# Optimization experiments

Measured on AMD Instinct MI355X. Metric: run time of the kernel, lower is better.

## Reference

```python
import jax, jax.numpy as jnp
import numpy as np

B, T, E = 8, 2048, 2048

def setup_inputs() -> dict:
    key = jax.random.key(0)
    k1, k2, k3 = jax.random.split(key, 3)
    x = jax.random.normal(k1, (B, T, E), dtype=jnp.float32)
    weight = jax.random.normal(k2, (T,), dtype=jnp.float32)
    bias = jax.random.normal(k3, (T,), dtype=jnp.float32)
    return {"x": x, "weight": weight, "bias": bias}

def _toeplitz_matrix(v, T):
    # M[i, j] = v[j - i] for j >= i, else 0  (upper-triangular Toeplitz)
    idx = jnp.arange(T)
    diff = idx[None, :] - idx[:, None]          # [T, T], diff = j - i
    M = jnp.where(diff >= 0, v[jnp.clip(diff, 0, T - 1)], jnp.zeros((), v.dtype))
    return M

def reference(x, weight, bias):
    Tlen = x.shape[1]
    W = _toeplitz_matrix(weight[:Tlen], Tlen).astype(x.dtype)  # [T, T]
    # original: out[b,e,t'] = sum_t x[b,e,t] * W[t,t']; in (B,T,E) layout:
    out = jnp.einsum('bte,ts->bse', x, W)
    out = out + bias[:Tlen][None, :, None]
    return out
```

## Files before the change

### kernel.cpp

```cpp
#include <hip/hip_runtime.h>
#include <hip/hip_bf16.h>

#define T_LEN 2048
#define E_LEN 2048
#define B_SZ  8
#define BM 128
#define BN 128
#define BK2 64
#define WREV_LEN 4104

typedef short short8 __attribute__((ext_vector_type(8)));
typedef float floatx4 __attribute__((ext_vector_type(4)));

typedef const __attribute__((address_space(1))) void* gas_ptr;
typedef __attribute__((address_space(3))) void* lds_ptr;

__global__ __launch_bounds__(256) void transpose_cast(
    const float* __restrict__ x, __hip_bfloat16* __restrict__ xT)
{
    const int t0 = blockIdx.x * 64, e0 = blockIdx.y * 64, b = blockIdx.z;
    __shared__ unsigned int W[64][33];
    const int tid = threadIdx.x;
    const int wave = tid >> 6, lane = tid & 63;

    const float* xb = x + (size_t)b * T_LEN * E_LEN;
    const int c = tid & 15;
    const int q = tid >> 4;

    #pragma unroll
    for (int i = 0; i < 2; ++i) {
        const int tp = q + 16 * i;
        const float4 a4 = *reinterpret_cast<const float4*>(
            xb + (size_t)(t0 + 2 * tp) * E_LEN + e0 + 4 * c);
        const float4 b4 = *reinterpret_cast<const float4*>(
            xb + (size_t)(t0 + 2 * tp + 1) * E_LEN + e0 + 4 * c);
        const float av[4] = {a4.x, a4.y, a4.z, a4.w};
        const float bv[4] = {b4.x, b4.y, b4.z, b4.w};
        #pragma unroll
        for (int j = 0; j < 4; ++j) {
            __hip_bfloat16 ha = __float2bfloat16(av[j]);
            __hip_bfloat16 hb = __float2bfloat16(bv[j]);
            unsigned int w =
                (unsigned int)*reinterpret_cast<unsigned short*>(&ha) |
                ((unsigned int)*reinterpret_cast<unsigned short*>(&hb) << 16);
            W[4 * c + j][tp] = w;
        }
    }
    __syncthreads();

    __hip_bfloat16* xTb = xT + (size_t)b * E_LEN * T_LEN;
    const int p = lane & 31;
    const int er = lane >> 5;
    #pragma unroll
    for (int i = 0; i < 8; ++i) {
        const int e = wave * 2 + i * 8 + er;
        unsigned int w = W[e][p];
        reinterpret_cast<unsigned int*>(
            xTb + (size_t)(e0 + e) * T_LEN + t0)[p] = w;
    }
}

__global__ __launch_bounds__(256) void build_wrevs(
    const float* __restrict__ w, __hip_bfloat16* __restrict__ wrevs)
{
    int total = 8 * WREV_LEN;
    for (int i = threadIdx.x + blockIdx.x * blockDim.x; i < total;
         i += blockDim.x * gridDim.x) {
        int p = i / WREV_LEN, q = i - p * WREV_LEN;
        int j = q + p;
        float v = (j < T_LEN) ? w[T_LEN - 1 - j] : 0.0f;
        wrevs[i] = __float2bfloat16(v);
    }
}

__global__ __launch_bounds__(256) void toeplitz_gemm(
    const __hip_bfloat16* __restrict__ xT,
    const __hip_bfloat16* __restrict__ wrevs,
    const float* __restrict__ bias,
    float* __restrict__ out)
{
    const int bx = blockIdx.x;
    const int mb = bx & 15, b = bx >> 4;
    const int nb = 15 - (int)blockIdx.y;
    const int e0 = mb * BM, s0 = nb * BN;
    const int tid = threadIdx.x;
    const int wave = tid >> 6, lane = tid & 63;
    const int wm = (wave & 1) * 64;
    const int wn = (wave >> 1) * 64;
    const int ln15 = lane & 15, quad = lane >> 4;

    __shared__ __hip_bfloat16 Atile[BM][BK2];

    floatx4 acc[4][4];
    #pragma unroll
    for (int i = 0; i < 4; ++i)
        #pragma unroll
        for (int j = 0; j < 4; ++j)
            acc[i][j] = (floatx4){0.f, 0.f, 0.f, 0.f};

    const int ktiles = (s0 + BN) / BK2;
    const __hip_bfloat16* xTb = xT + ((size_t)b * E_LEN + e0) * T_LEN;
    const short* wr = reinterpret_cast<const short*>(wrevs);
    char* AtileB = reinterpret_cast<char*>(&Atile[0][0]);

    for (int kt = 0; kt < ktiles; ++kt) {
        const int t0 = kt * BK2;
        __syncthreads();
        #pragma unroll
        for (int j = 0; j < 4; ++j) {
            const int c0 = (wave * 4 + j) * 64;
            const int c  = c0 + lane;
            const int r  = c >> 3, p = c & 7;
            const __hip_bfloat16* g = xTb + (size_t)r * T_LEN + t0 + p * 8;
            __builtin_amdgcn_global_load_lds(
                (gas_ptr)g, (lds_ptr)(AtileB + (size_t)c0 * 16), 16, 0, 0);
        }
        __syncthreads();

        #pragma unroll
        for (int kk = 0; kk < 2; ++kk) {
            short8 bfrag[4];
            #pragma unroll
            for (int ni = 0; ni < 4; ++ni) {
                int s = s0 + wn + ni * 16 + ln15;
                int C = (T_LEN - 1) - s + t0 + kk * 32 + quad * 8;
                int p = C & 7;
                bfrag[ni] = *reinterpret_cast<const short8*>(
                    wr + (size_t)p * WREV_LEN + (C - p));
            }
            short8 afrag[4];
            #pragma unroll
            for (int mi = 0; mi < 4; ++mi) {
                int r = wm + mi * 16 + ln15;
                afrag[mi] = *reinterpret_cast<const short8*>(
                    &Atile[r][kk * 32 + quad * 8]);
            }
            #pragma unroll
            for (int mi = 0; mi < 4; ++mi)
                #pragma unroll
                for (int ni = 0; ni < 4; ++ni)
                    acc[mi][ni] = __builtin_amdgcn_mfma_f32_16x16x32_bf16(
                        afrag[mi], bfrag[ni], acc[mi][ni], 0, 0, 0);
        }
    }

    #pragma unroll
    for (int ni = 0; ni < 4; ++ni) {
        int s = s0 + wn + ni * 16 + ln15;
        float bv = bias[s];
        #pragma unroll
        for (int mi = 0; mi < 4; ++mi) {
            int e = e0 + wm + mi * 16 + quad * 4;
            float* dst = out + ((size_t)b * T_LEN + s) * E_LEN + e;
            floatx4 v = acc[mi][ni];
            v.x += bv; v.y += bv; v.z += bv; v.w += bv;
            *reinterpret_cast<floatx4*>(dst) = v;
        }
    }
}

extern "C" void kernel_launch(void* const* d_in, const int* in_sizes, int n_in,
                              void* d_out, int out_size, void* d_ws, size_t ws_size,
                              hipStream_t stream)
{
    const float* x    = (const float*)d_in[0];
    const float* w    = (const float*)d_in[1];
    const float* bias = (const float*)d_in[2];
    float* out = (float*)d_out;

    __hip_bfloat16* xT = (__hip_bfloat16*)d_ws;
    __hip_bfloat16* wrevs =
        (__hip_bfloat16*)((char*)d_ws + (size_t)B_SZ * E_LEN * T_LEN * 2);

    transpose_cast<<<dim3(T_LEN / 64, E_LEN / 64, B_SZ), 256, 0, stream>>>(x, xT);
    build_wrevs<<<dim3(64), 256, 0, stream>>>(w, wrevs);
    toeplitz_gemm<<<dim3(16 * B_SZ, 16), 256, 0, stream>>>(xT, wrevs, bias, out);
}
```

Baseline: 335.6 us.

## Double-buffer LDS tile, swizzle A layout, and vectorize transpose stores

The GEMM now prefetches the next K tile into a second LDS buffer while computing on the current one, with one barrier per iteration instead of two. The A tile uses an XOR swizzle of 16-byte chunks to reduce LDS bank conflicts on fragment reads. The transpose kernel writes 16-byte vectors instead of 4-byte words. The costs are doubled LDS use, and correctness depends on the barrier waiting for the async global-to-LDS loads.

```diff
diff --git a/kernel.cpp b/kernel.cpp
--- a/kernel.cpp
+++ b/kernel.cpp
@@ -49,14 +49,19 @@
     __syncthreads();
 
     __hip_bfloat16* xTb = xT + (size_t)b * E_LEN * T_LEN;
-    const int p = lane & 31;
-    const int er = lane >> 5;
+    const int er = lane >> 3;
+    const int pc = (lane & 7) * 4;
     #pragma unroll
-    for (int i = 0; i < 8; ++i) {
-        const int e = wave * 2 + i * 8 + er;
-        unsigned int w = W[e][p];
-        reinterpret_cast<unsigned int*>(
-            xTb + (size_t)(e0 + e) * T_LEN + t0)[p] = w;
+    for (int i = 0; i < 2; ++i) {
+        const int e = wave * 8 + i * 32 + er;
+        uint4 v;
+        v.x = W[e][pc + 0];
+        v.y = W[e][pc + 1];
+        v.z = W[e][pc + 2];
+        v.w = W[e][pc + 3];
+        unsigned int* dst =
+            reinterpret_cast<unsigned int*>(xTb + (size_t)(e0 + e) * T_LEN + t0);
+        *reinterpret_cast<uint4*>(dst + pc) = v;
     }
 }
 
@@ -89,7 +94,7 @@
     const int wn = (wave >> 1) * 64;
     const int ln15 = lane & 15, quad = lane >> 4;
 
-    __shared__ __hip_bfloat16 Atile[BM][BK2];
+    __shared__ __hip_bfloat16 Atile[2][BM][BK2];
 
     floatx4 acc[4][4];
     #pragma unroll
@@ -101,21 +106,32 @@
     const int ktiles = (s0 + BN) / BK2;
     const __hip_bfloat16* xTb = xT + ((size_t)b * E_LEN + e0) * T_LEN;
     const short* wr = reinterpret_cast<const short*>(wrevs);
-    char* AtileB = reinterpret_cast<char*>(&Atile[0][0]);
+    char* AtileB = reinterpret_cast<char*>(&Atile[0][0][0]);
 
-    for (int kt = 0; kt < ktiles; ++kt) {
+    auto STAGE = [&](int buf, int kt) {
         const int t0 = kt * BK2;
-        __syncthreads();
         #pragma unroll
         for (int j = 0; j < 4; ++j) {
             const int c0 = (wave * 4 + j) * 64;
             const int c  = c0 + lane;
             const int r  = c >> 3, p = c & 7;
-            const __hip_bfloat16* g = xTb + (size_t)r * T_LEN + t0 + p * 8;
+            const int ps = p ^ (r & 7);
+            const __hip_bfloat16* g = xTb + (size_t)r * T_LEN + t0 + ps * 8;
             __builtin_amdgcn_global_load_lds(
-                (gas_ptr)g, (lds_ptr)(AtileB + (size_t)c0 * 16), 16, 0, 0);
+                (gas_ptr)g,
+                (lds_ptr)(AtileB + (size_t)buf * (BM * BK2 * 2) + c0 * 16),
+                16, 0, 0);
         }
-        __syncthreads();
+    };
+
+    STAGE(0, 0);
+    __syncthreads();
+    int cur = 0;
+
+    for (int kt = 0; kt < ktiles; ++kt) {
+        if (kt + 1 < ktiles) STAGE(cur ^ 1, kt + 1);
+        const int t0 = kt * BK2;
+        const char* Abuf = AtileB + (size_t)cur * (BM * BK2 * 2);
 
         #pragma unroll
         for (int kk = 0; kk < 2; ++kk) {
@@ -129,11 +145,12 @@
                     wr + (size_t)p * WREV_LEN + (C - p));
             }
             short8 afrag[4];
+            const int q = kk * 4 + quad;
             #pragma unroll
             for (int mi = 0; mi < 4; ++mi) {
                 int r = wm + mi * 16 + ln15;
-                afrag[mi] = *reinterpret_cast<const short8*>(
-                    &Atile[r][kk * 32 + quad * 8]);
+                int chunk = r * 8 + (q ^ (r & 7));
+                afrag[mi] = *reinterpret_cast<const short8*>(Abuf + chunk * 16);
             }
             #pragma unroll
             for (int mi = 0; mi < 4; ++mi)
@@ -142,6 +159,8 @@
                     acc[mi][ni] = __builtin_amdgcn_mfma_f32_16x16x32_bf16(
                         afrag[mi], bfrag[ni], acc[mi][ni], 0, 0, 0);
         }
+        __syncthreads();
+        cur ^= 1;
     }
 
     #pragma unroll
```

Measured after the change: 316.8 us. 5.6% less time.

## Fuse fp32 transpose-cast into Toeplitz GEMM with register-prefetched double-buffered LDS

Applied to the files above, without the earlier changes.

Removes the separate transpose_cast kernel and its bf16 workspace round trip. The GEMM now reads fp32 x directly, converts and transposes it into a double-buffered LDS tile, and prefetches the next k-tile into registers while MFMAs run on the current one. It also remaps block IDs so the blocks sharing an x panel are grouped for L2 locality, and adds an occupancy hint of 3 blocks per CU. The trade-off is that the GEMM reads x in fp32, which is twice the bytes per tile, and repeats the conversion work for every output column block, with extra register pressure and scalar LDS reads for the A fragments.

```diff
diff --git a/kernel.cpp b/kernel.cpp
--- a/kernel.cpp
+++ b/kernel.cpp
@@ -12,54 +12,6 @@
 typedef short short8 __attribute__((ext_vector_type(8)));
 typedef float floatx4 __attribute__((ext_vector_type(4)));
 
-typedef const __attribute__((address_space(1))) void* gas_ptr;
-typedef __attribute__((address_space(3))) void* lds_ptr;
-
-__global__ __launch_bounds__(256) void transpose_cast(
-    const float* __restrict__ x, __hip_bfloat16* __restrict__ xT)
-{
-    const int t0 = blockIdx.x * 64, e0 = blockIdx.y * 64, b = blockIdx.z;
-    __shared__ unsigned int W[64][33];
-    const int tid = threadIdx.x;
-    const int wave = tid >> 6, lane = tid & 63;
-
-    const float* xb = x + (size_t)b * T_LEN * E_LEN;
-    const int c = tid & 15;
-    const int q = tid >> 4;
-
-    #pragma unroll
-    for (int i = 0; i < 2; ++i) {
-        const int tp = q + 16 * i;
-        const float4 a4 = *reinterpret_cast<const float4*>(
-            xb + (size_t)(t0 + 2 * tp) * E_LEN + e0 + 4 * c);
-        const float4 b4 = *reinterpret_cast<const float4*>(
-            xb + (size_t)(t0 + 2 * tp + 1) * E_LEN + e0 + 4 * c);
-        const float av[4] = {a4.x, a4.y, a4.z, a4.w};
-        const float bv[4] = {b4.x, b4.y, b4.z, b4.w};
-        #pragma unroll
-        for (int j = 0; j < 4; ++j) {
-            __hip_bfloat16 ha = __float2bfloat16(av[j]);
-            __hip_bfloat16 hb = __float2bfloat16(bv[j]);
-            unsigned int w =
-                (unsigned int)*reinterpret_cast<unsigned short*>(&ha) |
-                ((unsigned int)*reinterpret_cast<unsigned short*>(&hb) << 16);
-            W[4 * c + j][tp] = w;
-        }
-    }
-    __syncthreads();
-
-    __hip_bfloat16* xTb = xT + (size_t)b * E_LEN * T_LEN;
-    const int p = lane & 31;
-    const int er = lane >> 5;
-    #pragma unroll
-    for (int i = 0; i < 8; ++i) {
-        const int e = wave * 2 + i * 8 + er;
-        unsigned int w = W[e][p];
-        reinterpret_cast<unsigned int*>(
-            xTb + (size_t)(e0 + e) * T_LEN + t0)[p] = w;
-    }
-}
-
 __global__ __launch_bounds__(256) void build_wrevs(
     const float* __restrict__ w, __hip_bfloat16* __restrict__ wrevs)
 {
@@ -73,15 +25,16 @@
     }
 }
 
-__global__ __launch_bounds__(256) void toeplitz_gemm(
-    const __hip_bfloat16* __restrict__ xT,
+__global__ __launch_bounds__(256, 3) void toeplitz_gemm_fused(
+    const float* __restrict__ x,
     const __hip_bfloat16* __restrict__ wrevs,
     const float* __restrict__ bias,
     float* __restrict__ out)
 {
-    const int bx = blockIdx.x;
-    const int mb = bx & 15, b = bx >> 4;
-    const int nb = 15 - (int)blockIdx.y;
+    const int lid = ((int)blockIdx.x & 7) * 256 + ((int)blockIdx.x >> 3);
+    const int nb = 15 - (lid & 15);
+    const int panel = lid >> 4;
+    const int mb = panel & 15, b = panel >> 4;
     const int e0 = mb * BM, s0 = nb * BN;
     const int tid = threadIdx.x;
     const int wave = tid >> 6, lane = tid & 63;
@@ -89,7 +42,7 @@
     const int wn = (wave >> 1) * 64;
     const int ln15 = lane & 15, quad = lane >> 4;
 
-    __shared__ __hip_bfloat16 Atile[BM][BK2];
+    __shared__ unsigned int W[2][BM][33];
 
     floatx4 acc[4][4];
     #pragma unroll
@@ -99,48 +52,89 @@
             acc[i][j] = (floatx4){0.f, 0.f, 0.f, 0.f};
 
     const int ktiles = (s0 + BN) / BK2;
-    const __hip_bfloat16* xTb = xT + ((size_t)b * E_LEN + e0) * T_LEN;
+    const float* xb = x + (size_t)b * T_LEN * E_LEN;
     const short* wr = reinterpret_cast<const short*>(wrevs);
-    char* AtileB = reinterpret_cast<char*>(&Atile[0][0]);
+
+    const int ec = tid & 31;
+    const int tr = wave * 2 + (lane >> 5);
+
+    float4 La[4], Lb[4];
+
+    auto LOADX = [&](int kt) {
+        const int t0 = kt * BK2;
+        #pragma unroll
+        for (int p2 = 0; p2 < 4; ++p2) {
+            const int tp = p2 * 8 + tr;
+            const float* g = xb + (size_t)(t0 + 2 * tp) * E_LEN + e0 + 4 * ec;
+            La[p2] = *reinterpret_cast<const float4*>(g);
+            Lb[p2] = *reinterpret_cast<const float4*>(g + E_LEN);
+        }
+    };
+    auto PACKWRITE = [&](int buf) {
+        #pragma unroll
+        for (int p2 = 0; p2 < 4; ++p2) {
+            const int tp = p2 * 8 + tr;
+            const float av[4] = {La[p2].x, La[p2].y, La[p2].z, La[p2].w};
+            const float bv[4] = {Lb[p2].x, Lb[p2].y, Lb[p2].z, Lb[p2].w};
+            #pragma unroll
+            for (int j = 0; j < 4; ++j) {
+                __hip_bfloat16 ha = __float2bfloat16(av[j]);
+                __hip_bfloat16 hb = __float2bfloat16(bv[j]);
+                unsigned int w =
+                    (unsigned int)*reinterpret_cast<unsigned short*>(&ha) |
+                    ((unsigned int)*reinterpret_cast<unsigned short*>(&hb) << 16);
+                W[buf][4 * ec + j][tp] = w;
+            }
+        }
+    };
+
+    LOADX(0);
+    PACKWRITE(0);
+    __syncthreads();
+    int cur = 0;
 
     for (int kt = 0; kt < ktiles; ++kt) {
         const int t0 = kt * BK2;
-        __syncthreads();
+
+        short8 bfrag[2][4];
         #pragma unroll
-        for (int j = 0; j < 4; ++j) {
-            const int c0 = (wave * 4 + j) * 64;
-            const int c  = c0 + lane;
-            const int r  = c >> 3, p = c & 7;
-            const __hip_bfloat16* g = xTb + (size_t)r * T_LEN + t0 + p * 8;
-            __builtin_amdgcn_global_load_lds(
-                (gas_ptr)g, (lds_ptr)(AtileB + (size_t)c0 * 16), 16, 0, 0);
-        }
-        __syncthreads();
-
-        #pragma unroll
-        for (int kk = 0; kk < 2; ++kk) {
-            short8 bfrag[4];
+        for (int kk = 0; kk < 2; ++kk)
             #pragma unroll
             for (int ni = 0; ni < 4; ++ni) {
                 int s = s0 + wn + ni * 16 + ln15;
                 int C = (T_LEN - 1) - s + t0 + kk * 32 + quad * 8;
                 int p = C & 7;
-                bfrag[ni] = *reinterpret_cast<const short8*>(
+                bfrag[kk][ni] = *reinterpret_cast<const short8*>(
                     wr + (size_t)p * WREV_LEN + (C - p));
             }
+
+        if (kt + 1 < ktiles) LOADX(kt + 1);
+
+        #pragma unroll
+        for (int kk = 0; kk < 2; ++kk) {
             short8 afrag[4];
             #pragma unroll
             for (int mi = 0; mi < 4; ++mi) {
-                int r = wm + mi * 16 + ln15;
-                afrag[mi] = *reinterpret_cast<const short8*>(
-                    &Atile[r][kk * 32 + quad * 8]);
+                const int r = wm + mi * 16 + ln15;
+                const unsigned int* Wr = &W[cur][r][kk * 16 + quad * 4];
+                union { unsigned int u[4]; short8 s8; } t;
+                t.u[0] = Wr[0]; t.u[1] = Wr[1];
+                t.u[2] = Wr[2]; t.u[3] = Wr[3];
+                afrag[mi] = t.s8;
             }
             #pragma unroll
             for (int mi = 0; mi < 4; ++mi)
                 #pragma unroll
                 for (int ni = 0; ni < 4; ++ni)
                     acc[mi][ni] = __builtin_amdgcn_mfma_f32_16x16x32_bf16(
-                        afrag[mi], bfrag[ni], acc[mi][ni], 0, 0, 0);
+                        afrag[mi], bfrag[kk][ni], acc[mi][ni], 0, 0, 0);
+        }
+
+        if (kt + 1 < ktiles) {
+            __syncthreads();
+            PACKWRITE(cur ^ 1);
+            __syncthreads();
+            cur ^= 1;
         }
     }
 
@@ -168,11 +162,8 @@
     const float* bias = (const float*)d_in[2];
     float* out = (float*)d_out;
 
-    __hip_bfloat16* xT = (__hip_bfloat16*)d_ws;
-    __hip_bfloat16* wrevs =
-        (__hip_bfloat16*)((char*)d_ws + (size_t)B_SZ * E_LEN * T_LEN * 2);
+    __hip_bfloat16* wrevs = (__hip_bfloat16*)d_ws;
 
-    transpose_cast<<<dim3(T_LEN / 64, E_LEN / 64, B_SZ), 256, 0, stream>>>(x, xT);
     build_wrevs<<<dim3(64), 256, 0, stream>>>(w, wrevs);
-    toeplitz_gemm<<<dim3(16 * B_SZ, 16), 256, 0, stream>>>(xT, wrevs, bias, out);
+    toeplitz_gemm_fused<<<dim3(2048), 256, 0, stream>>>(x, wrevs, bias, out);
 }
```

Result: slower. 485.7 us (+44.7%).
